# Performance work log

Measured on AMD Instinct MI355X. Metric: run time of the kernel, lower is better.

## Reference

```python
import jax, jax.numpy as jnp
import numpy as np

D_IN, D_ATT = 48, 8

def setup_inputs() -> dict:
    key = jax.random.key(0)
    k0, k1, k2, k3, k4 = jax.random.split(key, 5)
    N = 1048576
    x = jax.random.normal(k0, (N, D_IN), dtype=jnp.float32)
    # torch Linear weights have shape [out_features, in_features]
    Wk = jax.random.normal(k1, (D_ATT, D_IN), dtype=jnp.float32) * 0.1
    Wq = jax.random.normal(k2, (D_ATT, D_IN), dtype=jnp.float32) * 0.1
    Wv = jax.random.normal(k3, (D_ATT, D_IN), dtype=jnp.float32) * 0.1
    Wo = jax.random.normal(k4, (D_IN, D_ATT), dtype=jnp.float32) * 0.1
    return {"x": x, "Wk": Wk, "Wq": Wq, "Wv": Wv, "Wo": Wo}

def reference(x, Wk, Wq, Wv, Wo):
    # q, k, v: [N, 8]
    k = x @ Wk.T
    q = x @ Wq.T
    v = x @ Wv.T
    # attn: [8, 8] = q^T k / sqrt(8), softmax over dim=1 (columns)
    scores = (q.T @ k) / jnp.sqrt(jnp.float32(D_ATT))
    attn = jax.nn.softmax(scores, axis=1)
    # pre_output: [N, 8]; output: [N, 48]
    pre = v @ attn
    return pre @ Wo.T
```

## Files before the change

kernel.cpp:

```cpp
#include <hip/hip_runtime.h>
#include <hip/hip_bf16.h>


#define DI 48

typedef __attribute__((ext_vector_type(8))) short short8;
typedef __attribute__((ext_vector_type(4))) float f32x4;

__device__ inline unsigned int pack_bf16(float lo, float hi) {
  __hip_bfloat162 h = __float22bfloat162_rn(make_float2(lo, hi));
  return *reinterpret_cast<unsigned int*>(&h);
}

constexpr int GB = 512;
constexpr int SD = 36;

__global__ __launch_bounds__(256) void k_gram(const float* __restrict__ x,
                                              float* __restrict__ G, int N) {
  __shared__ unsigned int sh[4 * DI * SD];
  const int tid = threadIdx.x;
  const int wave = tid >> 6, lane = tid & 63;
  unsigned int* xt = &sh[wave * DI * SD];
  const int quad = lane >> 4, m = lane & 15;

  f32x4 acc[3][3] = {};

  const int rows_per_block = N / GB;
  const int rows_per_wave = rows_per_block / 4;
  const long long base0 = (long long)blockIdx.x * rows_per_block + wave * rows_per_wave;

  for (int tile = 0; tile < 8; ++tile) {
    const float* src = x + (base0 + tile * 64) * DI;
    float4 va[6], vb[6];
    int rp_[6], cg_[6];
#pragma unroll
    for (int s = 0; s < 6; ++s) {
      int task = lane + 64 * s;
      int rp = task / 12, cg = task % 12;
      rp_[s] = rp; cg_[s] = cg;
      const float4* p = (const float4*)(src + (2 * rp) * DI) + cg;
      va[s] = p[0];
      vb[s] = *(const float4*)((const float*)p + DI);
    }
#pragma unroll
    for (int s = 0; s < 6; ++s) {
      int rp = rp_[s], c0 = 4 * cg_[s];
      xt[(c0 + 0) * SD + rp] = pack_bf16(va[s].x, vb[s].x);
      xt[(c0 + 1) * SD + rp] = pack_bf16(va[s].y, vb[s].y);
      xt[(c0 + 2) * SD + rp] = pack_bf16(va[s].z, vb[s].z);
      xt[(c0 + 3) * SD + rp] = pack_bf16(va[s].w, vb[s].w);
    }
    asm volatile("s_waitcnt lgkmcnt(0)" ::: "memory");
#pragma unroll
    for (int kk = 0; kk < 2; ++kk) {
      short8 f[3];
#pragma unroll
      for (int t = 0; t < 3; ++t) {
        int c = 16 * t + m;
        f[t] = *(const short8*)&xt[c * SD + kk * 16 + quad * 4];
      }
#pragma unroll
      for (int i = 0; i < 3; ++i)
#pragma unroll
        for (int j = 0; j < 3; ++j)
          acc[i][j] = __builtin_amdgcn_mfma_f32_16x16x32_bf16(f[i], f[j], acc[i][j], 0, 0, 0);
    }
  }

  __syncthreads();
  float* red = (float*)sh;
  if (wave >= 2) {
    float* dst = red + (wave - 2) * 2304 + lane * 36;
#pragma unroll
    for (int i = 0; i < 3; ++i)
#pragma unroll
      for (int j = 0; j < 3; ++j)
#pragma unroll
        for (int r = 0; r < 4; ++r) dst[(i * 3 + j) * 4 + r] = acc[i][j][r];
  }
  __syncthreads();
  if (wave < 2) {
    const float* s2 = red + wave * 2304 + lane * 36;
#pragma unroll
    for (int i = 0; i < 3; ++i)
#pragma unroll
      for (int j = 0; j < 3; ++j)
#pragma unroll
        for (int r = 0; r < 4; ++r) acc[i][j][r] += s2[(i * 3 + j) * 4 + r];
  }
  __syncthreads();
  if (wave == 1) {
    float* dst = red + lane * 36;
#pragma unroll
    for (int i = 0; i < 3; ++i)
#pragma unroll
      for (int j = 0; j < 3; ++j)
#pragma unroll
        for (int r = 0; r < 4; ++r) dst[(i * 3 + j) * 4 + r] = acc[i][j][r];
  }
  __syncthreads();
  if (wave == 0) {
    const float* s1 = red + lane * 36;
#pragma unroll
    for (int i = 0; i < 3; ++i)
#pragma unroll
      for (int j = 0; j < 3; ++j)
#pragma unroll
        for (int r = 0; r < 4; ++r) {
          float v = acc[i][j][r] + s1[(i * 3 + j) * 4 + r];
          atomicAdd(&G[(16 * i + quad * 4 + r) * 48 + 16 * j + m], v);
        }
  }
}

__global__ void k_combine(const float* __restrict__ G,
                          const float* __restrict__ Wk,
                          const float* __restrict__ Wq,
                          const float* __restrict__ Wv,
                          const float* __restrict__ Wo,
                          __hip_bfloat16* __restrict__ Mt) {
  __shared__ float sG[2304];
  __shared__ float sWk[384], sWq[384], sWv[384], sWo[384];
  __shared__ float sU[384];
  __shared__ float sA[64];
  __shared__ float sP[384];
  const int t = threadIdx.x;

  for (int i = t; i < 2304; i += 256) sG[i] = G[i];
  for (int i = t; i < 384; i += 256) {
    sWk[i] = Wk[i]; sWq[i] = Wq[i]; sWv[i] = Wv[i]; sWo[i] = Wo[i];
  }
  __syncthreads();

  for (int e = t; e < 384; e += 256) {
    int q = e & 7, i = e >> 3;
    float s = 0.f;
#pragma unroll
    for (int j = 0; j < 48; ++j) s += sG[i * 48 + j] * sWk[q * 48 + j];
    sU[q * 48 + i] = s;
  }
  __syncthreads();

  if (t < 64) {
    int p = t >> 3, q = t & 7; (void)q;
    float s = 0.f;
#pragma unroll
    for (int i = 0; i < 48; ++i) s += sWq[p * 48 + i] * sU[(t & 7) * 48 + i];
    s *= 0.35355339059327373f;
    float mx = s;
    for (int d = 1; d < 8; d <<= 1) mx = fmaxf(mx, __shfl_xor(mx, d));
    float e = expf(s - mx);
    float den = e;
    for (int d = 1; d < 8; d <<= 1) den += __shfl_xor(den, d);
    sA[t] = e / den;
  }
  __syncthreads();

  for (int e = t; e < 384; e += 256) {
    int q = e & 7, i = e >> 3;
    float s = 0.f;
#pragma unroll
    for (int p = 0; p < 8; ++p) s += sWv[p * 48 + i] * sA[p * 8 + q];
    sP[i * 8 + q] = s;
  }
  __syncthreads();

  for (int e = t; e < 3072; e += 256) {
    int n = e >> 6, k = e & 63;
    float s = 0.f;
    if (k < 48) {
#pragma unroll
      for (int q = 0; q < 8; ++q) s += sP[k * 8 + q] * sWo[n * 8 + q];
    }
    Mt[e] = __float2bfloat16(s);
  }
}

__global__ __launch_bounds__(256) void k_out(const float* __restrict__ x,
                                             const __hip_bfloat16* __restrict__ Mt,
                                             float* __restrict__ out, int N) {
  __shared__ unsigned int sh[4 * 64 * SD];
  const int tid = threadIdx.x;
  const int wave = tid >> 6, lane = tid & 63;
  unsigned int* xs = &sh[wave * 64 * SD];
  const int quad = lane >> 4, m = lane & 15;

  short8 bf[2][3];
#pragma unroll
  for (int kk = 0; kk < 2; ++kk)
#pragma unroll
    for (int tn = 0; tn < 3; ++tn) {
      int n = 16 * tn + m;
      bf[kk][tn] = *(const short8*)((const short*)Mt + n * 64 + kk * 32 + quad * 8);
    }

#pragma unroll
  for (int s = 0; s < 8; ++s) {
    int d = lane + 64 * s;
    xs[(d >> 3) * SD + 24 + (d & 7)] = 0;
  }

  const int rows_per_block = N / GB;
  const int rows_per_wave = rows_per_block / 4;
  const long long base0 = (long long)blockIdx.x * rows_per_block + wave * rows_per_wave;

  for (int tile = 0; tile < 8; ++tile) {
    const long long rowt = base0 + tile * 64;
    const float* src = x + rowt * DI;
    float4 v[12];
    int r_[12], cg_[12];
#pragma unroll
    for (int s = 0; s < 12; ++s) {
      int task = lane + 64 * s;
      int r = task / 12, cg = task % 12;
      r_[s] = r; cg_[s] = cg;
      v[s] = *((const float4*)(src + r * DI) + cg);
    }
#pragma unroll
    for (int s = 0; s < 12; ++s) {
      int r = r_[s], cg = cg_[s];
      xs[r * SD + cg * 2]     = pack_bf16(v[s].x, v[s].y);
      xs[r * SD + cg * 2 + 1] = pack_bf16(v[s].z, v[s].w);
    }
    asm volatile("s_waitcnt lgkmcnt(0)" ::: "memory");
#pragma unroll
    for (int g = 0; g < 4; ++g) {
      f32x4 acc[3] = {};
#pragma unroll
      for (int kk = 0; kk < 2; ++kk) {
        short8 a = *(const short8*)&xs[(g * 16 + m) * SD + kk * 16 + quad * 4];
#pragma unroll
        for (int tn = 0; tn < 3; ++tn)
          acc[tn] = __builtin_amdgcn_mfma_f32_16x16x32_bf16(a, bf[kk][tn], acc[tn], 0, 0, 0);
      }
      float* orow = out + (rowt + g * 16) * DI;
#pragma unroll
      for (int tn = 0; tn < 3; ++tn)
#pragma unroll
        for (int r = 0; r < 4; ++r)
          orow[(quad * 4 + r) * DI + 16 * tn + m] = acc[tn][r];
    }
  }
}

extern "C" void kernel_launch(void* const* d_in, const int* in_sizes, int n_in,
                              void* d_out, int out_size, void* d_ws, size_t ws_size,
                              hipStream_t stream) {
  const float* x  = (const float*)d_in[0];
  const float* Wk = (const float*)d_in[1];
  const float* Wq = (const float*)d_in[2];
  const float* Wv = (const float*)d_in[3];
  const float* Wo = (const float*)d_in[4];
  float* out = (float*)d_out;
  const int N = in_sizes[0] / DI;

  float* G = (float*)d_ws;
  __hip_bfloat16* Mt = (__hip_bfloat16*)((char*)d_ws + 9216);

  hipMemsetAsync(G, 0, 2304 * sizeof(float), stream);
  k_gram<<<GB, 256, 0, stream>>>(x, G, N);
  k_combine<<<1, 256, 0, stream>>>(G, Wk, Wq, Wv, Wo, Mt);
  k_out<<<GB, 256, 0, stream>>>(x, Mt, out, N);
}
```

Before: 413.0 us.

## Compute v in gram pass and store bf16 v to avoid rereading x

```diff
diff --git a/kernel.cpp b/kernel.cpp
--- a/kernel.cpp
+++ b/kernel.cpp
@@ -12,29 +12,55 @@
   return *reinterpret_cast<unsigned int*>(&h);
 }
 
-constexpr int GB = 512;
-constexpr int SD = 36;
-
-__global__ __launch_bounds__(256) void k_gram(const float* __restrict__ x,
-                                              float* __restrict__ G, int N) {
-  __shared__ unsigned int sh[4 * DI * SD];
+constexpr int GB1 = 1024;
+constexpr int GB2 = 2048;
+constexpr int SDT = 20;
+constexpr int SDR = 28;
+constexpr int WDW = 48 * SDT + 32 * SDR;
+
+__global__ __launch_bounds__(256) void k_gram_v(const float* __restrict__ x,
+                                                const float* __restrict__ Wv,
+                                                float* __restrict__ G,
+                                                __hip_bfloat16* __restrict__ v,
+                                                int N) {
+  __shared__ unsigned int sh[4 * WDW];
   const int tid = threadIdx.x;
   const int wave = tid >> 6, lane = tid & 63;
-  unsigned int* xt = &sh[wave * DI * SD];
+  unsigned int* xt = &sh[wave * WDW];
+  unsigned int* xr = xt + 48 * SDT;
   const int quad = lane >> 4, m = lane & 15;
 
+  short8 wv0 = {}, wv1 = {};
+  if (m < 8) {
+    const float* wrow = Wv + m * DI + 8 * quad;
+    float4 c0 = *(const float4*)(wrow);
+    float4 c1 = *(const float4*)(wrow + 4);
+    unsigned int u0[4] = { pack_bf16(c0.x, c0.y), pack_bf16(c0.z, c0.w),
+                           pack_bf16(c1.x, c1.y), pack_bf16(c1.z, c1.w) };
+    wv0 = *(const short8*)u0;
+    if (quad < 2) {
+      float4 d0 = *(const float4*)(wrow + 32);
+      float4 d1 = *(const float4*)(wrow + 36);
+      unsigned int u1[4] = { pack_bf16(d0.x, d0.y), pack_bf16(d0.z, d0.w),
+                             pack_bf16(d1.x, d1.y), pack_bf16(d1.z, d1.w) };
+      wv1 = *(const short8*)u1;
+    }
+  }
+
   f32x4 acc[3][3] = {};
 
-  const int rows_per_block = N / GB;
-  const int rows_per_wave = rows_per_block / 4;
+  const int rows_per_block = N / GB1;
+  const int rows_per_wave = rows_per_block >> 2;
+  const int ntiles = rows_per_wave >> 5;
   const long long base0 = (long long)blockIdx.x * rows_per_block + wave * rows_per_wave;
 
-  for (int tile = 0; tile < 8; ++tile) {
-    const float* src = x + (base0 + tile * 64) * DI;
-    float4 va[6], vb[6];
-    int rp_[6], cg_[6];
-#pragma unroll
-    for (int s = 0; s < 6; ++s) {
+  for (int tile = 0; tile < ntiles; ++tile) {
+    const long long rowt = base0 + (long long)tile * 32;
+    const float* src = x + rowt * DI;
+    float4 va[3], vb[3];
+    int rp_[3], cg_[3];
+#pragma unroll
+    for (int s = 0; s < 3; ++s) {
       int task = lane + 64 * s;
       int rp = task / 12, cg = task % 12;
       rp_[s] = rp; cg_[s] = cg;
@@ -43,27 +69,41 @@
       vb[s] = *(const float4*)((const float*)p + DI);
     }
 #pragma unroll
-    for (int s = 0; s < 6; ++s) {
-      int rp = rp_[s], c0 = 4 * cg_[s];
-      xt[(c0 + 0) * SD + rp] = pack_bf16(va[s].x, vb[s].x);
-      xt[(c0 + 1) * SD + rp] = pack_bf16(va[s].y, vb[s].y);
-      xt[(c0 + 2) * SD + rp] = pack_bf16(va[s].z, vb[s].z);
-      xt[(c0 + 3) * SD + rp] = pack_bf16(va[s].w, vb[s].w);
+    for (int s = 0; s < 3; ++s) {
+      int rp = rp_[s], cg = cg_[s];
+      int c0 = 4 * cg;
+      xt[(c0 + 0) * SDT + rp] = pack_bf16(va[s].x, vb[s].x);
+      xt[(c0 + 1) * SDT + rp] = pack_bf16(va[s].y, vb[s].y);
+      xt[(c0 + 2) * SDT + rp] = pack_bf16(va[s].z, vb[s].z);
+      xt[(c0 + 3) * SDT + rp] = pack_bf16(va[s].w, vb[s].w);
+      unsigned int ra[2] = { pack_bf16(va[s].x, va[s].y), pack_bf16(va[s].z, va[s].w) };
+      unsigned int rb[2] = { pack_bf16(vb[s].x, vb[s].y), pack_bf16(vb[s].z, vb[s].w) };
+      *(uint2*)&xr[(2 * rp) * SDR + 2 * cg]     = *(const uint2*)ra;
+      *(uint2*)&xr[(2 * rp + 1) * SDR + 2 * cg] = *(const uint2*)rb;
     }
     asm volatile("s_waitcnt lgkmcnt(0)" ::: "memory");
-#pragma unroll
-    for (int kk = 0; kk < 2; ++kk) {
-      short8 f[3];
-#pragma unroll
-      for (int t = 0; t < 3; ++t) {
-        int c = 16 * t + m;
-        f[t] = *(const short8*)&xt[c * SD + kk * 16 + quad * 4];
+    short8 f[3];
+#pragma unroll
+    for (int t = 0; t < 3; ++t)
+      f[t] = *(const short8*)&xt[(16 * t + m) * SDT + quad * 4];
+#pragma unroll
+    for (int i = 0; i < 3; ++i)
+#pragma unroll
+      for (int j = 0; j < 3; ++j)
+        acc[i][j] = __builtin_amdgcn_mfma_f32_16x16x32_bf16(f[i], f[j], acc[i][j], 0, 0, 0);
+#pragma unroll
+    for (int g = 0; g < 2; ++g) {
+      short8 a0 = *(const short8*)&xr[(16 * g + m) * SDR + quad * 4];
+      short8 a1 = {};
+      if (quad < 2) a1 = *(const short8*)&xr[(16 * g + m) * SDR + 16 + quad * 4];
+      f32x4 vg = {};
+      vg = __builtin_amdgcn_mfma_f32_16x16x32_bf16(a0, wv0, vg, 0, 0, 0);
+      vg = __builtin_amdgcn_mfma_f32_16x16x32_bf16(a1, wv1, vg, 0, 0, 0);
+      if (m < 8) {
+        __hip_bfloat16* vr = v + (rowt + 16 * g + 4 * quad) * 8 + m;
+#pragma unroll
+        for (int r = 0; r < 4; ++r) vr[r * 8] = __float2bfloat16(vg[r]);
       }
-#pragma unroll
-      for (int i = 0; i < 3; ++i)
-#pragma unroll
-        for (int j = 0; j < 3; ++j)
-          acc[i][j] = __builtin_amdgcn_mfma_f32_16x16x32_bf16(f[i], f[j], acc[i][j], 0, 0, 0);
     }
   }
 
@@ -107,8 +147,8 @@
       for (int j = 0; j < 3; ++j)
 #pragma unroll
         for (int r = 0; r < 4; ++r) {
-          float v = acc[i][j][r] + s1[(i * 3 + j) * 4 + r];
-          atomicAdd(&G[(16 * i + quad * 4 + r) * 48 + 16 * j + m], v);
+          float val = acc[i][j][r] + s1[(i * 3 + j) * 4 + r];
+          atomicAdd(&G[(16 * i + quad * 4 + r) * 48 + 16 * j + m], val);
         }
   }
 }
@@ -116,19 +156,17 @@
 __global__ void k_combine(const float* __restrict__ G,
                           const float* __restrict__ Wk,
                           const float* __restrict__ Wq,
-                          const float* __restrict__ Wv,
                           const float* __restrict__ Wo,
-                          __hip_bfloat16* __restrict__ Mt) {
+                          __hip_bfloat16* __restrict__ Mt2) {
   __shared__ float sG[2304];
-  __shared__ float sWk[384], sWq[384], sWv[384], sWo[384];
+  __shared__ float sWk[384], sWq[384], sWo[384];
   __shared__ float sU[384];
   __shared__ float sA[64];
-  __shared__ float sP[384];
   const int t = threadIdx.x;
 
   for (int i = t; i < 2304; i += 256) sG[i] = G[i];
   for (int i = t; i < 384; i += 256) {
-    sWk[i] = Wk[i]; sWq[i] = Wq[i]; sWv[i] = Wv[i]; sWo[i] = Wo[i];
+    sWk[i] = Wk[i]; sWq[i] = Wq[i]; sWo[i] = Wo[i];
   }
   __syncthreads();
 
@@ -142,7 +180,7 @@
   __syncthreads();
 
   if (t < 64) {
-    int p = t >> 3, q = t & 7; (void)q;
+    int p = t >> 3;
     float s = 0.f;
 #pragma unroll
     for (int i = 0; i < 48; ++i) s += sWq[p * 48 + i] * sU[(t & 7) * 48 + i];
@@ -157,89 +195,47 @@
   __syncthreads();
 
   for (int e = t; e < 384; e += 256) {
-    int q = e & 7, i = e >> 3;
+    int p = e & 7, col = e >> 3;
     float s = 0.f;
 #pragma unroll
-    for (int p = 0; p < 8; ++p) s += sWv[p * 48 + i] * sA[p * 8 + q];
-    sP[i * 8 + q] = s;
-  }
-  __syncthreads();
-
-  for (int e = t; e < 3072; e += 256) {
-    int n = e >> 6, k = e & 63;
-    float s = 0.f;
-    if (k < 48) {
-#pragma unroll
-      for (int q = 0; q < 8; ++q) s += sP[k * 8 + q] * sWo[n * 8 + q];
-    }
-    Mt[e] = __float2bfloat16(s);
-  }
-}
-
-__global__ __launch_bounds__(256) void k_out(const float* __restrict__ x,
-                                             const __hip_bfloat16* __restrict__ Mt,
-                                             float* __restrict__ out, int N) {
-  __shared__ unsigned int sh[4 * 64 * SD];
+    for (int q = 0; q < 8; ++q) s += sA[p * 8 + q] * sWo[col * 8 + q];
+    Mt2[col * 8 + p] = __float2bfloat16(s);
+  }
+}
+
+__global__ __launch_bounds__(256) void k_out_v(const __hip_bfloat16* __restrict__ v,
+                                               const __hip_bfloat16* __restrict__ Mt2,
+                                               float* __restrict__ out, int N) {
   const int tid = threadIdx.x;
   const int wave = tid >> 6, lane = tid & 63;
-  unsigned int* xs = &sh[wave * 64 * SD];
   const int quad = lane >> 4, m = lane & 15;
 
-  short8 bf[2][3];
-#pragma unroll
-  for (int kk = 0; kk < 2; ++kk)
-#pragma unroll
-    for (int tn = 0; tn < 3; ++tn) {
-      int n = 16 * tn + m;
-      bf[kk][tn] = *(const short8*)((const short*)Mt + n * 64 + kk * 32 + quad * 8);
-    }
-
-#pragma unroll
-  for (int s = 0; s < 8; ++s) {
-    int d = lane + 64 * s;
-    xs[(d >> 3) * SD + 24 + (d & 7)] = 0;
-  }
-
-  const int rows_per_block = N / GB;
-  const int rows_per_wave = rows_per_block / 4;
-  const long long base0 = (long long)blockIdx.x * rows_per_block + wave * rows_per_wave;
-
-  for (int tile = 0; tile < 8; ++tile) {
-    const long long rowt = base0 + tile * 64;
-    const float* src = x + rowt * DI;
-    float4 v[12];
-    int r_[12], cg_[12];
-#pragma unroll
-    for (int s = 0; s < 12; ++s) {
-      int task = lane + 64 * s;
-      int r = task / 12, cg = task % 12;
-      r_[s] = r; cg_[s] = cg;
-      v[s] = *((const float4*)(src + r * DI) + cg);
-    }
-#pragma unroll
-    for (int s = 0; s < 12; ++s) {
-      int r = r_[s], cg = cg_[s];
-      xs[r * SD + cg * 2]     = pack_bf16(v[s].x, v[s].y);
-      xs[r * SD + cg * 2 + 1] = pack_bf16(v[s].z, v[s].w);
-    }
-    asm volatile("s_waitcnt lgkmcnt(0)" ::: "memory");
-#pragma unroll
-    for (int g = 0; g < 4; ++g) {
-      f32x4 acc[3] = {};
-#pragma unroll
-      for (int kk = 0; kk < 2; ++kk) {
-        short8 a = *(const short8*)&xs[(g * 16 + m) * SD + kk * 16 + quad * 4];
-#pragma unroll
-        for (int tn = 0; tn < 3; ++tn)
-          acc[tn] = __builtin_amdgcn_mfma_f32_16x16x32_bf16(a, bf[kk][tn], acc[tn], 0, 0, 0);
-      }
-      float* orow = out + (rowt + g * 16) * DI;
-#pragma unroll
-      for (int tn = 0; tn < 3; ++tn)
-#pragma unroll
-        for (int r = 0; r < 4; ++r)
-          orow[(quad * 4 + r) * DI + 16 * tn + m] = acc[tn][r];
-    }
+  short8 b[3] = {short8{}, short8{}, short8{}};
+  if (quad == 0) {
+#pragma unroll
+    for (int t = 0; t < 3; ++t)
+      b[t] = *(const short8*)(Mt2 + (16 * t + m) * 8);
+  }
+
+  const int rows_per_block = N / GB2;
+  const int rows_per_wave = rows_per_block >> 2;
+  const int ng = rows_per_wave >> 4;
+  const long long base = (long long)blockIdx.x * rows_per_block + wave * rows_per_wave;
+
+  for (int g = 0; g < ng; ++g) {
+    const long long rowg = base + (long long)g * 16;
+    short8 af = {};
+    if (quad == 0) af = *(const short8*)(v + (rowg + m) * 8);
+    f32x4 acc[3] = {};
+#pragma unroll
+    for (int t = 0; t < 3; ++t)
+      acc[t] = __builtin_amdgcn_mfma_f32_16x16x32_bf16(af, b[t], acc[t], 0, 0, 0);
+    float* orow = out + rowg * DI;
+#pragma unroll
+    for (int t = 0; t < 3; ++t)
+#pragma unroll
+      for (int r = 0; r < 4; ++r)
+        orow[(quad * 4 + r) * DI + 16 * t + m] = acc[t][r];
   }
 }
 
@@ -255,10 +251,11 @@
   const int N = in_sizes[0] / DI;
 
   float* G = (float*)d_ws;
-  __hip_bfloat16* Mt = (__hip_bfloat16*)((char*)d_ws + 9216);
+  __hip_bfloat16* Mt2 = (__hip_bfloat16*)((char*)d_ws + 9216);
+  __hip_bfloat16* v   = (__hip_bfloat16*)((char*)d_ws + 16384);
 
   hipMemsetAsync(G, 0, 2304 * sizeof(float), stream);
-  k_gram<<<GB, 256, 0, stream>>>(x, G, N);
-  k_combine<<<1, 256, 0, stream>>>(G, Wk, Wq, Wv, Wo, Mt);
-  k_out<<<GB, 256, 0, stream>>>(x, Mt, out, N);
-}
+  k_gram_v<<<GB1, 256, 0, stream>>>(x, Wv, G, v, N);
+  k_combine<<<1, 256, 0, stream>>>(G, Wk, Wq, Wo, Mt2);
+  k_out_v<<<GB2, 256, 0, stream>>>(v, Mt2, out, N);
+}
```

Measured after the change: 378.3 us. -8.4%, faster.
